# Kernel tuning notes

Measured on AMD Instinct MI355X. Metric: run time of the kernel, lower is better.

The kernel has to match this reference:

```python
import jax, jax.numpy as jnp
import numpy as np

N = 200000   # nodes
E = 600000   # directed edges
G = 8192     # graphs in batch
D_IN = 30
H = 128


def setup_inputs() -> dict:
    key = jax.random.key(0)
    ks = jax.random.split(key, 9)
    x = jax.random.normal(ks[0], (N, D_IN), jnp.float32)
    edge_index = jax.random.randint(ks[1], (2, E), 0, N, dtype=jnp.int32)
    batch_idx = jnp.sort(jax.random.randint(ks[2], (N,), 0, G, dtype=jnp.int32))
    W1 = jax.random.normal(ks[3], (D_IN, H), jnp.float32) / np.sqrt(D_IN)
    b1 = jnp.zeros((H,), jnp.float32)
    W2 = jax.random.normal(ks[4], (H, H), jnp.float32) / np.sqrt(H)
    b2 = jnp.zeros((H,), jnp.float32)
    W3 = jax.random.normal(ks[5], (H, H), jnp.float32) / np.sqrt(H)
    b3 = jnp.zeros((H,), jnp.float32)
    return {"x": x, "edge_index": edge_index, "batch_idx": batch_idx,
            "W1": W1, "b1": b1, "W2": W2, "b2": b2, "W3": W3, "b3": b3}


def _gcn_layer(x, W, b, src, dst, dinv):
    h = x @ W                                   # [N, H]
    norm = (dinv[src] * dinv[dst])[:, None]     # per-edge normalization
    msg = h[src] * norm                         # [E, H] gather + scale
    agg = jax.ops.segment_sum(msg, dst, num_segments=N)
    agg = agg + h * (dinv * dinv)[:, None]      # self-loop term, norm = 1/deg
    return jax.nn.relu(agg + b)


def reference(x, edge_index, batch_idx, W1, b1, W2, b2, W3, b3):
    src, dst = edge_index[0], edge_index[1]
    # degree with self-loops (edge weight 1), aggregated at target (col)
    deg = 1.0 + jax.ops.segment_sum(jnp.ones((E,), x.dtype), dst, num_segments=N)
    dinv = jax.lax.rsqrt(deg)                   # deg >= 1, safe
    h = _gcn_layer(x, W1, b1, src, dst, dinv)
    h = _gcn_layer(h, W2, b2, src, dst, dinv)
    h = _gcn_layer(h, W3, b3, src, dst, dinv)
    # global mean pool over batch segments
    sums = jax.ops.segment_sum(h, batch_idx, num_segments=G)
    counts = jax.ops.segment_sum(jnp.ones((N,), h.dtype), batch_idx, num_segments=G)
    return sums / jnp.maximum(counts, 1.0)[:, None]
```

## Files before the change

kernel.cpp:

```cpp
#include <hip/hip_runtime.h>


#define DIN 30
#define HD  128

typedef __attribute__((ext_vector_type(8))) short v8s;
typedef __attribute__((ext_vector_type(4))) float v4f;

static __device__ __forceinline__ unsigned short f2bf(float f) {
  unsigned int u = __float_as_uint(f);
  u += 0x7fffu + ((u >> 16) & 1u);
  return (unsigned short)(u >> 16);
}
static __device__ __forceinline__ float bf2f(unsigned short s) {
  return __uint_as_float(((unsigned int)s) << 16);
}
static __device__ __forceinline__ float bflo(unsigned int u) {
  return __uint_as_float(u << 16);
}
static __device__ __forceinline__ float bfhi(unsigned int u) {
  return __uint_as_float(u & 0xffff0000u);
}

static __device__ __forceinline__ void gload_lds16(const void* g, void* l) {
  __builtin_amdgcn_global_load_lds(
      (const __attribute__((address_space(1))) void*)g,
      (__attribute__((address_space(3))) void*)l, 16, 0, 0);
}

#define ACC8(v, s)                                            \
  {                                                           \
    a0 += (s) * (float)((v).x & 0xffu);                       \
    a1 += (s) * (float)(((v).x >> 8) & 0xffu);                \
    a2 += (s) * (float)(((v).x >> 16) & 0xffu);               \
    a3 += (s) * (float)((v).x >> 24);                         \
    a4 += (s) * (float)((v).y & 0xffu);                       \
    a5 += (s) * (float)(((v).y >> 8) & 0xffu);                \
    a6 += (s) * (float)(((v).y >> 16) & 0xffu);               \
    a7 += (s) * (float)((v).y >> 24);                         \
  }

__global__ void k_degree(const int* __restrict__ dst, int* __restrict__ deg,
                         int* __restrict__ eord, int E) {
  int e = blockIdx.x * blockDim.x + threadIdx.x;
  if (e < E) eord[e] = atomicAdd(&deg[dst[e]], 1);
}

__global__ void k_scan(const int* __restrict__ deg, int* __restrict__ scanbuf,
                       int* __restrict__ rowptr, float* __restrict__ dinv, int N) {
  __shared__ int s[256];
  __shared__ int sbase;
  int bid = blockIdx.x, tid = threadIdx.x;
  int base = bid * 1024 + tid * 4;
  int v[4]; int t = 0;
#pragma unroll
  for (int j = 0; j < 4; ++j) { int idx = base + j; v[j] = (idx < N) ? deg[idx] : 0; t += v[j]; }
  s[tid] = t; __syncthreads();
  for (int d = 1; d < 256; d <<= 1) {
    int u = (tid >= d) ? s[tid - d] : 0;
    __syncthreads();
    s[tid] += u;
    __syncthreads();
  }
  int myexcl = s[tid] - t;
  int blocktotal = s[255];
  if (tid == 0) atomicExch(&scanbuf[bid], blocktotal | 0x80000000);

  int pre = 0;
  for (int p = tid; p < bid; p += 256) {
    int val;
    do { val = atomicAdd(&scanbuf[p], 0); } while (!(val & 0x80000000));
    pre += val & 0x7fffffff;
  }
  __syncthreads();
  s[tid] = pre; __syncthreads();
  for (int d = 128; d > 0; d >>= 1) { if (tid < d) s[tid] += s[tid + d]; __syncthreads(); }
  if (tid == 0) sbase = s[0];
  __syncthreads();

  int run = sbase + myexcl;
#pragma unroll
  for (int j = 0; j < 4; ++j) {
    int idx = base + j;
    if (idx < N) {
      rowptr[idx] = run;
      dinv[idx] = rsqrtf((float)(1 + v[j]));
    }
    run += v[j];
    if (idx == N - 1) rowptr[N] = run;
  }
}

static __device__ __forceinline__ void wtf_one(const float* __restrict__ W,
                                               unsigned short* __restrict__ WTF,
                                               int idx, int Kreal, int KK) {
  int j = idx & 7;
  int c = idx >> 3;
  int l15 = c & 15;
  int quad = (c >> 4) & 3;
  int kk = (c >> 6) % KK;
  int t = c / (64 * KK);
  int k = kk * 32 + quad * 8 + j;
  int n = t * 16 + l15;
  WTF[idx] = (k < Kreal) ? f2bf(W[k * 128 + n]) : (unsigned short)0;
}

__global__ void k_prep(const int* __restrict__ src, const int* __restrict__ dst,
                       const int* __restrict__ rowptr, const int* __restrict__ eord,
                       int* __restrict__ col, int E,
                       const float* __restrict__ x, const float* __restrict__ dinv,
                       unsigned short* __restrict__ xb, int N,
                       const float* __restrict__ W1, const float* __restrict__ W2,
                       const float* __restrict__ W3,
                       unsigned short* __restrict__ W1F, unsigned short* __restrict__ W2F,
                       unsigned short* __restrict__ W3F,
                       const int* __restrict__ batch, int* __restrict__ gstart, int G,
                       float* __restrict__ out,
                       int SB, int XB, int WB, int BB) {
  int blk = blockIdx.x;
  if (blk < SB) {
    int e = blk * 256 + threadIdx.x;
    if (e < E) col[rowptr[dst[e]] + eord[e]] = src[e];
  } else if (blk < SB + XB) {
    int idx = (blk - SB) * 256 + threadIdx.x;
    if (idx < N * 4) {
      int n = idx >> 2, s4 = idx & 3, f0 = s4 * 8;
      float di = dinv[n];
      unsigned int w[4];
#pragma unroll
      for (int j = 0; j < 8; j += 2) {
        int f = f0 + j;
        float v0 = (f < DIN) ? x[(size_t)n * DIN + f] * di : 0.f;
        float v1 = (f + 1 < DIN) ? x[(size_t)n * DIN + f + 1] * di : 0.f;
        w[j >> 1] = (unsigned int)f2bf(v0) | ((unsigned int)f2bf(v1) << 16);
      }
      uint4 o; o.x = w[0]; o.y = w[1]; o.z = w[2]; o.w = w[3];
      ((uint4*)xb)[idx] = o;
    }
  } else if (blk < SB + XB + WB) {
    int idx = (blk - SB - XB) * 256 + threadIdx.x;
    if (idx < 4096) wtf_one(W1, W1F, idx, DIN, 1);
    else if (idx < 20480) wtf_one(W2, W2F, idx - 4096, 128, 4);
    else if (idx < 36864) wtf_one(W3, W3F, idx - 20480, 128, 4);
  } else if (blk < SB + XB + WB + BB) {
    int i = (blk - SB - XB - WB) * 256 + threadIdx.x;
    if (i >= N) return;
    int b = batch[i];
    int prev = (i == 0) ? -1 : batch[i - 1];
    for (int g = prev + 1; g <= b; ++g) gstart[g] = i;
    if (i == N - 1)
      for (int g = b + 1; g <= G; ++g) gstart[g] = N;
  } else {
    int idx = (blk - SB - XB - WB - BB) * 256 + threadIdx.x;
    if (idx < G * 32)
      ((float4*)out)[idx] = make_float4(0.f, 0.f, 0.f, 0.f);
  }
}

template <int K>
__global__ __launch_bounds__(256, 8) void k_fused(const void* __restrict__ hin,
                                                  const float* __restrict__ hscale,
                                                  const unsigned short* __restrict__ WTF,
                                                  const float* __restrict__ b,
                                                  const int* __restrict__ rowptr,
                                                  const int* __restrict__ col,
                                                  const float* __restrict__ dinv,
                                                  unsigned char* __restrict__ Cq,
                                                  float* __restrict__ Cs, int N) {
  constexpr int KK = K / 32;
  constexpr int KP = (K == 128) ? 136 : 40;
  constexpr int CP = 132;
  constexpr int SMSZ = (16 * KP > 16 * CP) ? 16 * KP : 16 * CP;
  constexpr int CH = 64;
  constexpr int RB = (K == 128) ? 128 : 64;
  __shared__ __align__(16) unsigned short sm[SMSZ];
  __shared__ __align__(16) unsigned char stg[CH * RB];
  __shared__ int smcol[CH];
  __shared__ float sscale[(K == 128) ? CH : 1];

  int tid = threadIdx.x;
  int l16 = tid & 15;
  int g = tid >> 4;
  int lane = tid & 63, wv = tid >> 6, quad = lane >> 4, l15 = lane & 15;
  int row0 = blockIdx.x * 16;
  int node = row0 + g;
  int rend = row0 + 16; if (rend > N) rend = N;

  float a0 = 0.f, a1 = 0.f, a2 = 0.f, a3 = 0.f, a4 = 0.f, a5 = 0.f, a6 = 0.f, a7 = 0.f;
  int e0 = 0, e1 = 0; float di = 0.f;
  if (node < N) {
    e0 = rowptr[node]; e1 = rowptr[node + 1]; di = dinv[node];
    if constexpr (K == 32) {
      unsigned int u = ((const unsigned int*)hin)[(size_t)node * 16 + l16];
      a0 = bflo(u); a1 = bfhi(u);
    } else {
      uint2 u = ((const uint2*)hin)[(size_t)node * 16 + l16];
      float s = hscale[node];
      ACC8(u, s);
    }
  }
  int eb = rowptr[row0];
  int ee = rowptr[rend];

  for (int c0 = eb; c0 < ee; c0 += CH) {
    if (tid < CH) {
      int e = c0 + tid;
      int c = (e < ee) ? col[e] : 0;
      smcol[tid] = c;
      if constexpr (K == 128) sscale[tid] = hscale[c];
    }
    __syncthreads();
    if constexpr (K == 128) {
#pragma unroll
      for (int q = 0; q < 2; ++q) {
        int slb = wv * 16 + q * 8;
        int row = smcol[slb + (lane >> 3)];
        const unsigned char* gp = (const unsigned char*)hin + (size_t)row * 128 + (lane & 7) * 16;
        gload_lds16(gp, &stg[slb * 128]);
      }
    } else {
      int slb = wv * 16;
      int row = smcol[slb + (lane >> 2)];
      const unsigned short* gp = (const unsigned short*)hin + (size_t)row * 32 + (lane & 3) * 8;
      gload_lds16(gp, &stg[slb * 64]);
    }
    __syncthreads();
    int lo = (e0 > c0) ? e0 : c0;
    int hi = (e1 < c0 + CH) ? e1 : (c0 + CH);
    int e2 = lo;
    for (; e2 + 2 <= hi; e2 += 2) {
      int i0 = e2 - c0, i1 = i0 + 1;
      if constexpr (K == 32) {
        unsigned int w0 = *(const unsigned int*)&stg[i0 * 64 + l16 * 4];
        unsigned int w1 = *(const unsigned int*)&stg[i1 * 64 + l16 * 4];
        a0 += bflo(w0); a1 += bfhi(w0);
        a0 += bflo(w1); a1 += bfhi(w1);
      } else {
        uint2 w0 = *(const uint2*)&stg[i0 * 128 + l16 * 8];
        uint2 w1 = *(const uint2*)&stg[i1 * 128 + l16 * 8];
        float s0 = sscale[i0], s1 = sscale[i1];
        ACC8(w0, s0);
        ACC8(w1, s1);
      }
    }
    if (e2 < hi) {
      int i0 = e2 - c0;
      if constexpr (K == 32) {
        unsigned int w0 = *(const unsigned int*)&stg[i0 * 64 + l16 * 4];
        a0 += bflo(w0); a1 += bfhi(w0);
      } else {
        uint2 w0 = *(const uint2*)&stg[i0 * 128 + l16 * 8];
        float s0 = sscale[i0];
        ACC8(w0, s0);
      }
    }
    __syncthreads();
  }

  if constexpr (K == 32) {
    *(unsigned int*)&sm[g * KP + l16 * 2] =
        (unsigned int)f2bf(a0 * di) | ((unsigned int)f2bf(a1 * di) << 16);
  } else {
    uint4 o;
    o.x = (unsigned int)f2bf(a0 * di) | ((unsigned int)f2bf(a1 * di) << 16);
    o.y = (unsigned int)f2bf(a2 * di) | ((unsigned int)f2bf(a3 * di) << 16);
    o.z = (unsigned int)f2bf(a4 * di) | ((unsigned int)f2bf(a5 * di) << 16);
    o.w = (unsigned int)f2bf(a6 * di) | ((unsigned int)f2bf(a7 * di) << 16);
    *(uint4*)&sm[g * KP + l16 * 8] = o;
  }
  __syncthreads();

  v8s af[KK];
#pragma unroll
  for (int kk = 0; kk < KK; ++kk)
    af[kk] = *(const v8s*)&sm[l15 * KP + kk * 32 + quad * 8];
  __syncthreads();

  int crow0 = row0 + quad * 4;
  float dr[4];
  if (crow0 + 3 < N) {
    float4 d4 = *(const float4*)&dinv[crow0];
    dr[0] = d4.x; dr[1] = d4.y; dr[2] = d4.z; dr[3] = d4.w;
  } else {
#pragma unroll
    for (int i = 0; i < 4; ++i) dr[i] = (crow0 + i < N) ? dinv[crow0 + i] : 0.f;
  }

#pragma unroll
  for (int tt = 0; tt < 2; ++tt) {
    int t = wv * 2 + tt;
    v4f acc = {0.f, 0.f, 0.f, 0.f};
#pragma unroll
    for (int kk = 0; kk < KK; ++kk) {
      v8s bf = *(const v8s*)(WTF + (size_t)(((t * KK + kk) * 4 + quad) * 16 + l15) * 8);
      acc = __builtin_amdgcn_mfma_f32_16x16x32_bf16(af[kk], bf, acc, 0, 0, 0);
    }
    float bias = b[t * 16 + l15];
#pragma unroll
    for (int i = 0; i < 4; ++i) {
      float o = fmaxf(acc[i] + bias, 0.f) * dr[i];
      sm[(quad * 4 + i) * CP + t * 16 + l15] = f2bf(o);
    }
  }
  __syncthreads();

  {
    uint4 u = *(const uint4*)&sm[g * CP + l16 * 8];
    float f0 = bflo(u.x), f1 = bfhi(u.x), f2 = bflo(u.y), f3 = bfhi(u.y);
    float f4 = bflo(u.z), f5 = bfhi(u.z), f6 = bflo(u.w), f7 = bfhi(u.w);
    float m = fmaxf(fmaxf(fmaxf(f0, f1), fmaxf(f2, f3)),
                    fmaxf(fmaxf(f4, f5), fmaxf(f6, f7)));
    m = fmaxf(m, __shfl_xor(m, 1));
    m = fmaxf(m, __shfl_xor(m, 2));
    m = fmaxf(m, __shfl_xor(m, 4));
    m = fmaxf(m, __shfl_xor(m, 8));
    float inv = (m > 0.f) ? 255.f / m : 0.f;
    unsigned q0 = (unsigned)__float2int_rn(fminf(f0 * inv, 255.f));
    unsigned q1 = (unsigned)__float2int_rn(fminf(f1 * inv, 255.f));
    unsigned q2 = (unsigned)__float2int_rn(fminf(f2 * inv, 255.f));
    unsigned q3 = (unsigned)__float2int_rn(fminf(f3 * inv, 255.f));
    unsigned q4 = (unsigned)__float2int_rn(fminf(f4 * inv, 255.f));
    unsigned q5 = (unsigned)__float2int_rn(fminf(f5 * inv, 255.f));
    unsigned q6 = (unsigned)__float2int_rn(fminf(f6 * inv, 255.f));
    unsigned q7 = (unsigned)__float2int_rn(fminf(f7 * inv, 255.f));
    uint2 o;
    o.x = q0 | (q1 << 8) | (q2 << 16) | (q3 << 24);
    o.y = q4 | (q5 << 8) | (q6 << 16) | (q7 << 24);
    int row = row0 + g;
    if (row < N) {
      ((uint2*)Cq)[(size_t)row * 16 + l16] = o;
      if (l16 == 0) Cs[row] = m * (1.f / 255.f);
    }
  }
}

__global__ __launch_bounds__(256, 8) void k_fused_pool(const unsigned char* __restrict__ hin,
                                                       const float* __restrict__ hscale,
                                                       const unsigned short* __restrict__ WTF,
                                                       const float* __restrict__ b,
                                                       const int* __restrict__ rowptr,
                                                       const int* __restrict__ col,
                                                       const float* __restrict__ dinv,
                                                       const int* __restrict__ batch,
                                                       float* __restrict__ out, int N) {
  constexpr int KK = 4, KP = 136, CP = 132;
  constexpr int SMSZ = 16 * KP;
  constexpr int CH = 64;
  __shared__ __align__(16) unsigned short sm[SMSZ];
  __shared__ __align__(16) unsigned char stg[CH * 128];
  __shared__ int smcol[CH];
  __shared__ float sscale[CH];
  __shared__ int sbatch[16];

  int tid = threadIdx.x;
  int l16 = tid & 15;
  int g = tid >> 4;
  int lane = tid & 63, wv = tid >> 6, quad = lane >> 4, l15 = lane & 15;
  int row0 = blockIdx.x * 16;
  int node = row0 + g;
  int rend = row0 + 16; if (rend > N) rend = N;

  if (tid < 16) sbatch[tid] = (row0 + tid < N) ? batch[row0 + tid] : -1;

  float a0 = 0.f, a1 = 0.f, a2 = 0.f, a3 = 0.f, a4 = 0.f, a5 = 0.f, a6 = 0.f, a7 = 0.f;
  int e0 = 0, e1 = 0; float di = 0.f;
  if (node < N) {
    e0 = rowptr[node]; e1 = rowptr[node + 1]; di = dinv[node];
    uint2 u = ((const uint2*)hin)[(size_t)node * 16 + l16];
    float s = hscale[node];
    ACC8(u, s);
  }
  int eb = rowptr[row0];
  int ee = rowptr[rend];

  for (int c0 = eb; c0 < ee; c0 += CH) {
    if (tid < CH) {
      int e = c0 + tid;
      int c = (e < ee) ? col[e] : 0;
      smcol[tid] = c;
      sscale[tid] = hscale[c];
    }
    __syncthreads();
#pragma unroll
    for (int q = 0; q < 2; ++q) {
      int slb = wv * 16 + q * 8;
      int row = smcol[slb + (lane >> 3)];
      const unsigned char* gp = hin + (size_t)row * 128 + (lane & 7) * 16;
      gload_lds16(gp, &stg[slb * 128]);
    }
    __syncthreads();
    int lo = (e0 > c0) ? e0 : c0;
    int hi = (e1 < c0 + CH) ? e1 : (c0 + CH);
    int e2 = lo;
    for (; e2 + 2 <= hi; e2 += 2) {
      int i0 = e2 - c0, i1 = i0 + 1;
      uint2 w0 = *(const uint2*)&stg[i0 * 128 + l16 * 8];
      uint2 w1 = *(const uint2*)&stg[i1 * 128 + l16 * 8];
      float s0 = sscale[i0], s1 = sscale[i1];
      ACC8(w0, s0);
      ACC8(w1, s1);
    }
    if (e2 < hi) {
      int i0 = e2 - c0;
      uint2 w0 = *(const uint2*)&stg[i0 * 128 + l16 * 8];
      float s0 = sscale[i0];
      ACC8(w0, s0);
    }
    __syncthreads();
  }

  {
    uint4 o;
    o.x = (unsigned int)f2bf(a0 * di) | ((unsigned int)f2bf(a1 * di) << 16);
    o.y = (unsigned int)f2bf(a2 * di) | ((unsigned int)f2bf(a3 * di) << 16);
    o.z = (unsigned int)f2bf(a4 * di) | ((unsigned int)f2bf(a5 * di) << 16);
    o.w = (unsigned int)f2bf(a6 * di) | ((unsigned int)f2bf(a7 * di) << 16);
    *(uint4*)&sm[g * KP + l16 * 8] = o;
  }
  __syncthreads();

  v8s af[KK];
#pragma unroll
  for (int kk = 0; kk < KK; ++kk)
    af[kk] = *(const v8s*)&sm[l15 * KP + kk * 32 + quad * 8];
  __syncthreads();

#pragma unroll
  for (int tt = 0; tt < 2; ++tt) {
    int t = wv * 2 + tt;
    v4f acc = {0.f, 0.f, 0.f, 0.f};
#pragma unroll
    for (int kk = 0; kk < KK; ++kk) {
      v8s bf = *(const v8s*)(WTF + (size_t)(((t * KK + kk) * 4 + quad) * 16 + l15) * 8);
      acc = __builtin_amdgcn_mfma_f32_16x16x32_bf16(af[kk], bf, acc, 0, 0, 0);
    }
    float bias = b[t * 16 + l15];
#pragma unroll
    for (int i = 0; i < 4; ++i) {
      float o = fmaxf(acc[i] + bias, 0.f);
      sm[(quad * 4 + i) * CP + t * 16 + l15] = f2bf(o);
    }
  }
  __syncthreads();

  int f = tid & 127;
  int grp = tid >> 7;
  float run = 0.f;
  int cur = -1;
#pragma unroll
  for (int j = 0; j < 8; ++j) {
    int r = grp * 8 + j;
    int gg = sbatch[r];
    if (gg != cur) {
      if (cur >= 0) atomicAdd(&out[(size_t)cur * 128 + f], run);
      run = 0.f; cur = gg;
    }
    if (gg >= 0) run += bf2f(sm[r * CP + f]);
  }
  if (cur >= 0) atomicAdd(&out[(size_t)cur * 128 + f], run);
}

__global__ void k_finalize(float* __restrict__ out, const int* __restrict__ gstart, int G) {
  int idx = blockIdx.x * blockDim.x + threadIdx.x;
  if (idx >= G * 128) return;
  int g = idx >> 7;
  float cnt = (float)(gstart[g + 1] - gstart[g]);
  out[idx] = out[idx] / fmaxf(cnt, 1.f);
}

extern "C" void kernel_launch(void* const* d_in, const int* in_sizes, int n_in,
                              void* d_out, int out_size, void* d_ws, size_t ws_size,
                              hipStream_t stream) {
  const float* x  = (const float*)d_in[0];
  const int* ei   = (const int*)d_in[1];
  const int* batch = (const int*)d_in[2];
  const float* W1 = (const float*)d_in[3];
  const float* b1 = (const float*)d_in[4];
  const float* W2 = (const float*)d_in[5];
  const float* b2 = (const float*)d_in[6];
  const float* W3 = (const float*)d_in[7];
  const float* b3 = (const float*)d_in[8];
  float* out = (float*)d_out;
  int N = in_sizes[2];
  int E = in_sizes[1] / 2;
  int G = out_size / HD;
  const int* src = ei;
  const int* dst = ei + E;

  size_t off = 0;
  char* ws = (char*)d_ws;
  auto alloc = [&](size_t bytes) -> void* {
    void* p = ws + off;
    off += (bytes + 255) & ~(size_t)255;
    return p;
  };
  int nb1024 = (N + 1023) / 1024;
  int*   deg     = (int*)alloc((size_t)N * 4);
  int*   scanbuf = (int*)alloc((size_t)nb1024 * 4);
  float* dinv    = (float*)alloc((size_t)N * 4);
  int*   rowptr  = (int*)alloc((size_t)(N + 1) * 4);
  int*   eord    = (int*)alloc((size_t)E * 4);
  int*   col     = (int*)alloc((size_t)E * 4);
  int*   gstart  = (int*)alloc((size_t)(G + 1) * 4);
  unsigned short* xb  = (unsigned short*)alloc((size_t)N * 32 * 2);
  unsigned char*  hAq = (unsigned char*)alloc((size_t)N * 128);
  float*          hAs = (float*)alloc((size_t)N * 4);
  unsigned char*  hBq = (unsigned char*)alloc((size_t)N * 128);
  float*          hBs = (float*)alloc((size_t)N * 4);
  unsigned short* W1F = (unsigned short*)alloc(4096 * 2);
  unsigned short* W2F = (unsigned short*)alloc(16384 * 2);
  unsigned short* W3F = (unsigned short*)alloc(16384 * 2);
  (void)ws_size; (void)n_in;

  size_t zbytes = (size_t)((char*)dinv - (char*)deg);
  hipMemsetAsync(deg, 0, zbytes, stream);
  k_degree<<<(E + 255) / 256, 256, 0, stream>>>(dst, deg, eord, E);
  k_scan<<<nb1024, 256, 0, stream>>>(deg, scanbuf, rowptr, dinv, N);

  int SB = (E + 255) / 256;
  int XB = (N * 4 + 255) / 256;
  int WB = 144;
  int BB = (N + 255) / 256;
  int ZB = (G * 32 + 255) / 256;
  k_prep<<<SB + XB + WB + BB + ZB, 256, 0, stream>>>(src, dst, rowptr, eord, col, E,
                                                     x, dinv, xb, N,
                                                     W1, W2, W3, W1F, W2F, W3F,
                                                     batch, gstart, G, out,
                                                     SB, XB, WB, BB);

  int fusedBlocks = (N + 15) / 16;
  k_fused<32><<<fusedBlocks, 256, 0, stream>>>(xb, nullptr, W1F, b1, rowptr, col, dinv,
                                               hAq, hAs, N);
  k_fused<128><<<fusedBlocks, 256, 0, stream>>>(hAq, hAs, W2F, b2, rowptr, col, dinv,
                                                hBq, hBs, N);
  k_fused_pool<<<fusedBlocks, 256, 0, stream>>>(hBq, hBs, W3F, b3, rowptr, col, dinv,
                                                batch, out, N);
  k_finalize<<<(G * 128 + 255) / 256, 256, 0, stream>>>(out, gstart, G);
}
```

Before: 237.5 us.

## Split neighbor gathering per wavefront to drop block-wide barriers

The edge-gather loop used to work on 64-edge chunks covering the whole 16-node block, with three __syncthreads per chunk. Now each wavefront handles the edge range of its own 4 nodes in 32-edge chunks, using private LDS slots for column indices, scales and staged rows. Block barriers are removed from the loop, so waves no longer stall on each other's load imbalance. The K=128 staging buffer doubles in size and the launch-bounds occupancy hint drops from 8 to 7. Correctness now depends on in-wave ordering of the LDS and async global-to-LDS writes without an explicit wait before the reads.

```diff
diff --git a/kernel.cpp b/kernel.cpp
--- a/kernel.cpp
+++ b/kernel.cpp
@@ -158,7 +158,7 @@
 }
 
 template <int K>
-__global__ __launch_bounds__(256, 8) void k_fused(const void* __restrict__ hin,
+__global__ __launch_bounds__(256, 7) void k_fused(const void* __restrict__ hin,
                                                   const float* __restrict__ hscale,
                                                   const unsigned short* __restrict__ WTF,
                                                   const float* __restrict__ b,
@@ -171,12 +171,12 @@
   constexpr int KP = (K == 128) ? 136 : 40;
   constexpr int CP = 132;
   constexpr int SMSZ = (16 * KP > 16 * CP) ? 16 * KP : 16 * CP;
-  constexpr int CH = 64;
+  constexpr int WCAP = 32;
   constexpr int RB = (K == 128) ? 128 : 64;
   __shared__ __align__(16) unsigned short sm[SMSZ];
-  __shared__ __align__(16) unsigned char stg[CH * RB];
-  __shared__ int smcol[CH];
-  __shared__ float sscale[(K == 128) ? CH : 1];
+  __shared__ __align__(16) unsigned char stg[4 * WCAP * RB];
+  __shared__ int scol[4 * WCAP];
+  __shared__ float swsc[(K == 128) ? 4 * WCAP : 1];
 
   int tid = threadIdx.x;
   int l16 = tid & 15;
@@ -184,7 +184,6 @@
   int lane = tid & 63, wv = tid >> 6, quad = lane >> 4, l15 = lane & 15;
   int row0 = blockIdx.x * 16;
   int node = row0 + g;
-  int rend = row0 + 16; if (rend > N) rend = N;
 
   float a0 = 0.f, a1 = 0.f, a2 = 0.f, a3 = 0.f, a4 = 0.f, a5 = 0.f, a6 = 0.f, a7 = 0.f;
   int e0 = 0, e1 = 0; float di = 0.f;
@@ -199,37 +198,41 @@
       ACC8(u, s);
     }
   }
-  int eb = rowptr[row0];
-  int ee = rowptr[rend];
-
-  for (int c0 = eb; c0 < ee; c0 += CH) {
-    if (tid < CH) {
-      int e = c0 + tid;
-      int c = (e < ee) ? col[e] : 0;
-      smcol[tid] = c;
-      if constexpr (K == 128) sscale[tid] = hscale[c];
-    }
-    __syncthreads();
+  int nb0 = row0 + wv * 4; if (nb0 > N) nb0 = N;
+  int nb1 = nb0 + 4; if (nb1 > N - nb0 + nb0) nb1 = nb1;
+  nb1 = row0 + wv * 4 + 4; if (nb1 > N) nb1 = N;
+  int web = rowptr[nb0];
+  int wee = rowptr[nb1];
+
+  for (int c0 = web; c0 < wee; c0 += WCAP) {
+    if (lane < WCAP) {
+      int e = c0 + lane;
+      int c = (e < wee) ? col[e] : 0;
+      scol[wv * WCAP + lane] = c;
+      if constexpr (K == 128) swsc[wv * WCAP + lane] = hscale[c];
+    }
     if constexpr (K == 128) {
 #pragma unroll
-      for (int q = 0; q < 2; ++q) {
-        int slb = wv * 16 + q * 8;
-        int row = smcol[slb + (lane >> 3)];
+      for (int q = 0; q < 4; ++q) {
+        int slot = q * 8 + (lane >> 3);
+        int row = scol[wv * WCAP + slot];
         const unsigned char* gp = (const unsigned char*)hin + (size_t)row * 128 + (lane & 7) * 16;
-        gload_lds16(gp, &stg[slb * 128]);
+        gload_lds16(gp, &stg[(wv * WCAP + slot) * 128]);
       }
     } else {
-      int slb = wv * 16;
-      int row = smcol[slb + (lane >> 2)];
-      const unsigned short* gp = (const unsigned short*)hin + (size_t)row * 32 + (lane & 3) * 8;
-      gload_lds16(gp, &stg[slb * 64]);
-    }
-    __syncthreads();
+#pragma unroll
+      for (int q = 0; q < 2; ++q) {
+        int slot = q * 16 + (lane >> 2);
+        int row = scol[wv * WCAP + slot];
+        const unsigned short* gp = (const unsigned short*)hin + (size_t)row * 32 + (lane & 3) * 8;
+        gload_lds16(gp, &stg[(wv * WCAP + slot) * 64]);
+      }
+    }
     int lo = (e0 > c0) ? e0 : c0;
-    int hi = (e1 < c0 + CH) ? e1 : (c0 + CH);
+    int hi = (e1 < c0 + WCAP) ? e1 : (c0 + WCAP);
     int e2 = lo;
     for (; e2 + 2 <= hi; e2 += 2) {
-      int i0 = e2 - c0, i1 = i0 + 1;
+      int i0 = wv * WCAP + (e2 - c0), i1 = i0 + 1;
       if constexpr (K == 32) {
         unsigned int w0 = *(const unsigned int*)&stg[i0 * 64 + l16 * 4];
         unsigned int w1 = *(const unsigned int*)&stg[i1 * 64 + l16 * 4];
@@ -238,23 +241,22 @@
       } else {
         uint2 w0 = *(const uint2*)&stg[i0 * 128 + l16 * 8];
         uint2 w1 = *(const uint2*)&stg[i1 * 128 + l16 * 8];
-        float s0 = sscale[i0], s1 = sscale[i1];
+        float s0 = swsc[i0], s1 = swsc[i1];
         ACC8(w0, s0);
         ACC8(w1, s1);
       }
     }
     if (e2 < hi) {
-      int i0 = e2 - c0;
+      int i0 = wv * WCAP + (e2 - c0);
       if constexpr (K == 32) {
         unsigned int w0 = *(const unsigned int*)&stg[i0 * 64 + l16 * 4];
         a0 += bflo(w0); a1 += bfhi(w0);
       } else {
         uint2 w0 = *(const uint2*)&stg[i0 * 128 + l16 * 8];
-        float s0 = sscale[i0];
+        float s0 = swsc[i0];
         ACC8(w0, s0);
       }
     }
-    __syncthreads();
   }
 
   if constexpr (K == 32) {
@@ -334,7 +336,7 @@
   }
 }
 
-__global__ __launch_bounds__(256, 8) void k_fused_pool(const unsigned char* __restrict__ hin,
+__global__ __launch_bounds__(256, 7) void k_fused_pool(const unsigned char* __restrict__ hin,
                                                        const float* __restrict__ hscale,
                                                        const unsigned short* __restrict__ WTF,
                                                        const float* __restrict__ b,
@@ -345,11 +347,11 @@
                                                        float* __restrict__ out, int N) {
   constexpr int KK = 4, KP = 136, CP = 132;
   constexpr int SMSZ = 16 * KP;
-  constexpr int CH = 64;
+  constexpr int WCAP = 32;
   __shared__ __align__(16) unsigned short sm[SMSZ];
-  __shared__ __align__(16) unsigned char stg[CH * 128];
-  __shared__ int smcol[CH];
-  __shared__ float sscale[CH];
+  __shared__ __align__(16) unsigned char stg[4 * WCAP * 128];
+  __shared__ int scol[4 * WCAP];
+  __shared__ float swsc[4 * WCAP];
   __shared__ int sbatch[16];
 
   int tid = threadIdx.x;
@@ -358,7 +360,6 @@
   int lane = tid & 63, wv = tid >> 6, quad = lane >> 4, l15 = lane & 15;
   int row0 = blockIdx.x * 16;
   int node = row0 + g;
-  int rend = row0 + 16; if (rend > N) rend = N;
 
   if (tid < 16) sbatch[tid] = (row0 + tid < N) ? batch[row0 + tid] : -1;
 
@@ -370,43 +371,42 @@
     float s = hscale[node];
     ACC8(u, s);
   }
-  int eb = rowptr[row0];
-  int ee = rowptr[rend];
-
-  for (int c0 = eb; c0 < ee; c0 += CH) {
-    if (tid < CH) {
-      int e = c0 + tid;
-      int c = (e < ee) ? col[e] : 0;
-      smcol[tid] = c;
-      sscale[tid] = hscale[c];
-    }
-    __syncthreads();
-#pragma unroll
-    for (int q = 0; q < 2; ++q) {
-      int slb = wv * 16 + q * 8;
-      int row = smcol[slb + (lane >> 3)];
+  int nb0 = row0 + wv * 4; if (nb0 > N) nb0 = N;
+  int nb1 = row0 + wv * 4 + 4; if (nb1 > N) nb1 = N;
+  int web = rowptr[nb0];
+  int wee = rowptr[nb1];
+
+  for (int c0 = web; c0 < wee; c0 += WCAP) {
+    if (lane < WCAP) {
+      int e = c0 + lane;
+      int c = (e < wee) ? col[e] : 0;
+      scol[wv * WCAP + lane] = c;
+      swsc[wv * WCAP + lane] = hscale[c];
+    }
+#pragma unroll
+    for (int q = 0; q < 4; ++q) {
+      int slot = q * 8 + (lane >> 3);
+      int row = scol[wv * WCAP + slot];
       const unsigned char* gp = hin + (size_t)row * 128 + (lane & 7) * 16;
-      gload_lds16(gp, &stg[slb * 128]);
-    }
-    __syncthreads();
+      gload_lds16(gp, &stg[(wv * WCAP + slot) * 128]);
+    }
     int lo = (e0 > c0) ? e0 : c0;
-    int hi = (e1 < c0 + CH) ? e1 : (c0 + CH);
+    int hi = (e1 < c0 + WCAP) ? e1 : (c0 + WCAP);
     int e2 = lo;
     for (; e2 + 2 <= hi; e2 += 2) {
-      int i0 = e2 - c0, i1 = i0 + 1;
+      int i0 = wv * WCAP + (e2 - c0), i1 = i0 + 1;
       uint2 w0 = *(const uint2*)&stg[i0 * 128 + l16 * 8];
       uint2 w1 = *(const uint2*)&stg[i1 * 128 + l16 * 8];
-      float s0 = sscale[i0], s1 = sscale[i1];
+      float s0 = swsc[i0], s1 = swsc[i1];
       ACC8(w0, s0);
       ACC8(w1, s1);
     }
     if (e2 < hi) {
-      int i0 = e2 - c0;
+      int i0 = wv * WCAP + (e2 - c0);
       uint2 w0 = *(const uint2*)&stg[i0 * 128 + l16 * 8];
-      float s0 = sscale[i0];
+      float s0 = swsc[i0];
       ACC8(w0, s0);
     }
-    __syncthreads();
   }
 
   {
```

After: 250.7 us. 5.5% more time.
